# Performance work log

Measured on AMD Instinct MI355X. Metric: run time of the kernel, lower is better.

Reference implementation:

```python
import jax, jax.numpy as jnp
import numpy as np

NB = 8            # num_blocks
D = 128           # embed_dim
D_INNER = 256     # expand=2
HEADS = 4
P = 64            # headdim
N = 32            # d_state
K = 4             # d_conv
CONV_DIM = D_INNER + 2 * N          # 320 (x, B, C streams)
D_IN_PROJ = 2 * D_INNER + 2 * N + HEADS  # 580 (z, xBC, dt)


def setup_inputs():
    key = jax.random.key(0)
    ks = iter(jax.random.split(key, 16))
    f = lambda shape, s=0.02: (jax.random.normal(next(ks), shape, jnp.float32) * s)
    B, L = 2, 4096
    return {
        'x': jax.random.normal(next(ks), (B, L, D), jnp.float32),
        'residual': jnp.zeros((B, L, D), jnp.float32),
        'ln1_w': jnp.ones((NB, D)), 'ln1_b': jnp.zeros((NB, D)),
        'ln2_w': jnp.ones((NB, D)), 'ln2_b': jnp.zeros((NB, D)),
        'fc1_w': f((NB, 4 * D, D)), 'fc1_b': jnp.zeros((NB, 4 * D)),
        'fc2_w': f((NB, D, 2 * D)), 'fc2_b': jnp.zeros((NB, D)),
        'in_proj_w': f((NB, D_IN_PROJ, D)),
        'conv_w': f((NB, CONV_DIM, K), 0.1), 'conv_b': jnp.zeros((NB, CONV_DIM)),
        'dt_bias': f((NB, HEADS), 0.1),
        'A_log': jnp.tile(jnp.log(jnp.arange(1, HEADS + 1, dtype=jnp.float32)), (NB, 1)),
        'Dp': jnp.ones((NB, HEADS)),
        'rms_w': jnp.ones((NB, D_INNER)),
        'out_proj_w': f((NB, D, D_INNER)),
        'h': 64, 'w': 64,
    }


def layernorm(x, w, b):
    mu = jnp.mean(x, -1, keepdims=True)
    var = jnp.mean((x - mu) ** 2, -1, keepdims=True)
    return (x - mu) * jax.lax.rsqrt(var + 1e-5) * w + b


def mamba2(x, in_proj_w, conv_w, conv_b, dt_bias, A_log, Dp, rms_w, out_proj_w):
    Bb, L, _ = x.shape
    zxbcdt = jnp.einsum('bld,ed->ble', x, in_proj_w)          # [B,L,580]
    z = zxbcdt[..., :D_INNER]
    xBC = zxbcdt[..., D_INNER:D_INNER + CONV_DIM]
    dt = jax.nn.softplus(zxbcdt[..., -HEADS:] + dt_bias)      # [B,L,H]
    # causal depthwise conv1d + silu
    xc = jnp.moveaxis(xBC, 1, 2)                              # [B,C,L]
    xc = jax.lax.conv_general_dilated(xc, conv_w[:, None, :], (1,), [(K - 1, 0)],
                                      feature_group_count=CONV_DIM)
    xBC = jax.nn.silu(jnp.moveaxis(xc, 1, 2) + conv_b)
    xs = xBC[..., :D_INNER].reshape(Bb, L, HEADS, P)          # [B,L,H,P]
    Bm = xBC[..., D_INNER:D_INNER + N]                        # [B,L,N]
    Cm = xBC[..., D_INNER + N:]                               # [B,L,N]
    dA = jnp.exp(dt * (-jnp.exp(A_log)))                      # [B,L,H]

    def step(hst, inp):
        dA_t, dt_t, B_t, C_t, x_t = inp
        hst = hst * dA_t[:, :, None, None] + (dt_t[:, :, None, None] * x_t[..., None]) * B_t[:, None, None, :]
        return hst, jnp.einsum('bhpn,bn->bhp', hst, C_t)

    tfirst = lambda a: jnp.moveaxis(a, 1, 0)
    h0 = jnp.zeros((Bb, HEADS, P, N), x.dtype)
    _, ys = jax.lax.scan(step, h0, (tfirst(dA), tfirst(dt), tfirst(Bm), tfirst(Cm), tfirst(xs)))
    y = jnp.moveaxis(ys, 0, 1) + Dp[None, None, :, None] * xs # [B,L,H,P]
    y = y.reshape(Bb, L, D_INNER) * jax.nn.silu(z)            # gated
    y = y * jax.lax.rsqrt(jnp.mean(y * y, -1, keepdims=True) + 1e-5) * rms_w
    return jnp.einsum('be,de->bd'.replace('b', 'bl'), y, out_proj_w)


def mlp(x, fc1_w, fc1_b, fc2_w, fc2_b):
    x12 = jnp.einsum('bld,ed->ble', x, fc1_w) + fc1_b
    x1, x2 = jnp.split(x12, 2, axis=-1)
    return jnp.einsum('ble,de->bld', jax.nn.silu(x1) * x2, fc2_w) + fc2_b


def reference(x, residual, ln1_w, ln1_b, ln2_w, ln2_b, fc1_w, fc1_b, fc2_w, fc2_b,
              in_proj_w, conv_w, conv_b, dt_bias, A_log, Dp, rms_w, out_proj_w, h, w):
    for i in range(NB):
        residual = x
        x1 = layernorm(residual, ln1_w[i], ln1_b[i])
        x_m = residual + mamba2(x1, in_proj_w[i], conv_w[i], conv_b[i], dt_bias[i],
                                A_log[i], Dp[i], rms_w[i], out_proj_w[i])
        residual = x_m
        x2 = layernorm(residual, ln2_w[i], ln2_b[i])
        x = residual + mlp(x2, fc1_w[i], fc1_b[i], fc2_w[i], fc2_b[i])
    return (x, residual)
```

## Files before the change

### kernel.cpp

```cpp
#include <hip/hip_runtime.h>
#include <hip/hip_bf16.h>
#include <cstddef>

#define NBLK 8
#define DD   128
#define DI   256
#define NH   4
#define PP   64
#define NNs  32
#define CONVD 320
#define EE   580
#define BB   2
#define LLEN 4096
#define ML   (BB*LLEN)
#define SEGS 256
#define TT   16
#define GPAD 264

typedef unsigned short u16;
typedef short bf16x8 __attribute__((ext_vector_type(8)));
typedef float f32x4 __attribute__((ext_vector_type(4)));

__device__ __forceinline__ float siluf(float x){ return x / (1.f + expf(-x)); }
__device__ __forceinline__ float b2f(u16 u){ return __uint_as_float((unsigned)u << 16); }
__device__ __forceinline__ u16 f2b(float f){
    __hip_bfloat16 h = __float2bfloat16(f);
    return *reinterpret_cast<u16*>(&h);
}
__device__ __forceinline__ void ld8f(const u16* p, float* f){
    ushort4 a = *(const ushort4*)p;
    ushort4 b = *(const ushort4*)(p + 4);
    f[0]=b2f(a.x); f[1]=b2f(a.y); f[2]=b2f(a.z); f[3]=b2f(a.w);
    f[4]=b2f(b.x); f[5]=b2f(b.y); f[6]=b2f(b.z); f[7]=b2f(b.w);
}

#define IPW_N (NBLK*EE*DD)
#define OPW_N (NBLK*DD*DI)
#define F1W_N (NBLK*512*DD)
#define F2W_N (NBLK*DD*DI)
#define CVT_TOT (IPW_N+OPW_N+F1W_N+F2W_N)

__global__ __launch_bounds__(256) void cvt_weights(const float* __restrict__ ip,
                                                   const float* __restrict__ op,
                                                   const float* __restrict__ f1,
                                                   const float* __restrict__ f2,
                                                   const float* __restrict__ xin,
                                                   u16* __restrict__ dip,
                                                   u16* __restrict__ dop,
                                                   u16* __restrict__ df1,
                                                   u16* __restrict__ df2,
                                                   float* __restrict__ xout)
{
    int i = blockIdx.x * 256 + threadIdx.x;
    if (i < IPW_N)                          dip[i] = f2b(ip[i]);
    else if (i < IPW_N + OPW_N)             dop[i - IPW_N] = f2b(op[i - IPW_N]);
    else if (i < IPW_N + OPW_N + F1W_N)     df1[i - IPW_N - OPW_N] = f2b(f1[i - IPW_N - OPW_N]);
    else                                    df2[i - IPW_N - OPW_N - F1W_N] = f2b(f2[i - IPW_N - OPW_N - F1W_N]);
    if (i < ML * DD) xout[i] = xin[i];
}

__global__ __launch_bounds__(256) void inproj_ln_gemm(const float* __restrict__ X,
                                                      const float* __restrict__ lnw,
                                                      const float* __restrict__ lnb,
                                                      const u16* __restrict__ W,
                                                      u16* __restrict__ C)
{
    __shared__ __align__(16) u16 Ash[64*128];
    __shared__ __align__(16) u16 Wsh[64*128];
    __shared__ float red[64][8];
    const int tid = threadIdx.x;
    const int wave = tid >> 6, lane = tid & 63;
    const int l15 = lane & 15, quad = lane >> 4;
    const int bm = blockIdx.y * 64;
    const int bn = blockIdx.x * 64;
    const int lrow = tid >> 2, sub = tid & 3;

#pragma unroll
    for (int i = 0; i < 4; i++) {
        int k8 = sub + 4*i;
        uint4 wv = make_uint4(0u,0u,0u,0u);
        if (bn + lrow < EE)
            wv = *(const uint4*)(W + (size_t)(bn + lrow) * DD + k8*8);
        *(uint4*)&Wsh[((size_t)k8*64 + lrow) * 8] = wv;
    }

    const float* xr = X + (size_t)(bm + lrow) * DD + sub*32;
    float4 xv[8];
    float ps = 0.f, pq = 0.f;
#pragma unroll
    for (int i = 0; i < 8; i++) {
        xv[i] = *(const float4*)(xr + i*4);
        ps += xv[i].x + xv[i].y + xv[i].z + xv[i].w;
        pq += xv[i].x*xv[i].x + xv[i].y*xv[i].y + xv[i].z*xv[i].z + xv[i].w*xv[i].w;
    }
    red[lrow][sub] = ps; red[lrow][4+sub] = pq;
    __syncthreads();
    float s = red[lrow][0]+red[lrow][1]+red[lrow][2]+red[lrow][3];
    float q = red[lrow][4]+red[lrow][5]+red[lrow][6]+red[lrow][7];
    float mu = s * (1.f/DD);
    float rstd = rsqrtf(q*(1.f/DD) - mu*mu + 1e-5f);
#pragma unroll
    for (int i = 0; i < 4; i++) {
        float4 a0 = xv[2*i], a1 = xv[2*i+1];
        int c0 = sub*32 + i*8;
        u16 o[8];
        o[0] = f2b((a0.x-mu)*rstd*lnw[c0+0] + lnb[c0+0]);
        o[1] = f2b((a0.y-mu)*rstd*lnw[c0+1] + lnb[c0+1]);
        o[2] = f2b((a0.z-mu)*rstd*lnw[c0+2] + lnb[c0+2]);
        o[3] = f2b((a0.w-mu)*rstd*lnw[c0+3] + lnb[c0+3]);
        o[4] = f2b((a1.x-mu)*rstd*lnw[c0+4] + lnb[c0+4]);
        o[5] = f2b((a1.y-mu)*rstd*lnw[c0+5] + lnb[c0+5]);
        o[6] = f2b((a1.z-mu)*rstd*lnw[c0+6] + lnb[c0+6]);
        o[7] = f2b((a1.w-mu)*rstd*lnw[c0+7] + lnb[c0+7]);
        *(uint4*)&Ash[((size_t)(sub*4+i)*64 + lrow) * 8] = *(uint4*)o;
    }
    __syncthreads();

    f32x4 acc[4];
#pragma unroll
    for (int nt = 0; nt < 4; nt++) acc[nt] = (f32x4){0.f,0.f,0.f,0.f};
#pragma unroll
    for (int kk = 0; kk < 4; kk++) {
        bf16x8 af = *(const bf16x8*)&Ash[(((kk*4 + quad)*64) + wave*16 + l15) * 8];
#pragma unroll
        for (int nt = 0; nt < 4; nt++) {
            bf16x8 bfv = *(const bf16x8*)&Wsh[(((kk*4 + quad)*64) + nt*16 + l15) * 8];
            acc[nt] = __builtin_amdgcn_mfma_f32_16x16x32_bf16(af, bfv, acc[nt], 0, 0, 0);
        }
    }
#pragma unroll
    for (int nt = 0; nt < 4; nt++) {
        int n = bn + nt*16 + l15;
        if (n < EE) {
#pragma unroll
            for (int r = 0; r < 4; r++) {
                int m = bm + wave*16 + quad*4 + r;
                C[(size_t)m * EE + n] = f2b(acc[nt][r]);
            }
        }
    }
}

__global__ __launch_bounds__(256) void scan1(const u16* __restrict__ zx,
                                             const float* __restrict__ cw,
                                             const float* __restrict__ cb,
                                             const float* __restrict__ dt_bias,
                                             const float* __restrict__ A_log,
                                             float* __restrict__ seg,
                                             float* __restrict__ segsum)
{
    __shared__ float Bsh[4][TT*NNs];
    __shared__ float dts[4][TT], das[4][TT];
    int wv = threadIdx.x >> 6;
    int p = threadIdx.x & 63;
    int sg = blockIdx.x % (SEGS/4);
    int bh = blockIdx.x / (SEGS/4);
    int h = bh % NH;
    int b = bh / NH;
    int s = sg*4 + wv;
    int l0 = s * TT;
    int row0 = b * LLEN + l0;

    float xr[TT+3];
    const u16* xcol = zx + (size_t)row0 * EE + 256 + h*64 + p;
#pragma unroll
    for (int r = 0; r < TT+3; r++) {
        int l = l0 - 3 + r;
        xr[r] = (l >= 0) ? b2f(xcol[(ptrdiff_t)(r-3) * EE]) : 0.f;
    }
    float4 wx = *(const float4*)(cw + (size_t)(h*64+p) * 4);
    float cbx = cb[h*64+p];

    if (p < NNs) {
        float br[TT+3];
        const u16* bcol = zx + (size_t)row0 * EE + 512 + p;
#pragma unroll
        for (int r = 0; r < TT+3; r++) {
            int l = l0 - 3 + r;
            br[r] = (l >= 0) ? b2f(bcol[(ptrdiff_t)(r-3) * EE]) : 0.f;
        }
        float4 wb = *(const float4*)(cw + (size_t)(256+p) * 4);
        float cbb = cb[256+p];
#pragma unroll
        for (int t = 0; t < TT; t++)
            Bsh[wv][t*NNs + p] = siluf(cbb + wb.x*br[t] + wb.y*br[t+1] + wb.z*br[t+2] + wb.w*br[t+3]);
    }
    if (p < TT) {
        float v = b2f(zx[(size_t)(row0+p)*EE + (EE-NH) + h]) + dt_bias[h];
        float dt = (v > 20.f) ? v : log1pf(expf(v));
        dts[wv][p] = dt;
        das[wv][p] = expf(-expf(A_log[h]) * dt);
    }
    __syncthreads();

    float hreg[NNs];
#pragma unroll
    for (int n = 0; n < NNs; n++) hreg[n] = 0.f;
    float sdt = 0.f;
#pragma unroll
    for (int t = 0; t < TT; t++) {
        float dA = das[wv][t];
        float dt = dts[wv][t];
        float xv = siluf(cbx + wx.x*xr[t] + wx.y*xr[t+1] + wx.z*xr[t+2] + wx.w*xr[t+3]);
        float dtx = dt * xv;
#pragma unroll
        for (int n4 = 0; n4 < 8; n4++) {
            float4 Bv = *(const float4*)&Bsh[wv][t*NNs + n4*4];
            hreg[n4*4+0] = fmaf(hreg[n4*4+0], dA, dtx * Bv.x);
            hreg[n4*4+1] = fmaf(hreg[n4*4+1], dA, dtx * Bv.y);
            hreg[n4*4+2] = fmaf(hreg[n4*4+2], dA, dtx * Bv.z);
            hreg[n4*4+3] = fmaf(hreg[n4*4+3], dA, dtx * Bv.w);
        }
        sdt += dt;
    }
    int bidg = bh * SEGS + s;
    float* dst = seg + ((size_t)bidg * PP + p) * NNs;
#pragma unroll
    for (int n4 = 0; n4 < 8; n4++)
        *(float4*)(dst + n4*4) = make_float4(hreg[n4*4+0], hreg[n4*4+1], hreg[n4*4+2], hreg[n4*4+3]);
    if (p == 0) segsum[bidg] = sdt;
}

__global__ __launch_bounds__(256) void scan2(float* __restrict__ seg,
                                             const float* __restrict__ segsum,
                                             const float* __restrict__ A_log)
{
    int bh = blockIdx.x >> 3;
    int chunk = blockIdx.x & 7;
    int h = bh % NH;
    int entry = chunk * 256 + threadIdx.x;
    float negA = -expf(A_log[h]);
    float hs = 0.f;
    const float* ss = segsum + bh * SEGS;
    float* base = seg + (size_t)bh * SEGS * (PP * NNs) + entry;
    for (int j0 = 0; j0 < SEGS; j0 += 16) {
        float e[16], a[16];
#pragma unroll
        for (int k = 0; k < 16; k++) {
            a[k] = ss[j0 + k];
            e[k] = base[(size_t)(j0 + k) * (PP * NNs)];
        }
#pragma unroll
        for (int k = 0; k < 16; k++) {
            float Aj = expf(negA * a[k]);
            base[(size_t)(j0 + k) * (PP * NNs)] = hs;
            hs = fmaf(Aj, hs, e[k]);
        }
    }
}

__global__ __launch_bounds__(256) void scan3(const u16* __restrict__ zx,
                                             const float* __restrict__ cw,
                                             const float* __restrict__ cb,
                                             const float* __restrict__ dt_bias,
                                             const float* __restrict__ A_log,
                                             const float* __restrict__ seg,
                                             const float* __restrict__ Dp,
                                             u16* __restrict__ y)
{
    __shared__ float BCsh[4][TT*64];
    __shared__ float dts[4][TT], das[4][TT];
    int wv = threadIdx.x >> 6;
    int p = threadIdx.x & 63;
    int sg = blockIdx.x % (SEGS/4);
    int bh = blockIdx.x / (SEGS/4);
    int h = bh % NH;
    int b = bh / NH;
    int s = sg*4 + wv;
    int l0 = s * TT;
    int row0 = b * LLEN + l0;

    float xr[TT+3];
    const u16* xcol = zx + (size_t)row0 * EE + 256 + h*64 + p;
#pragma unroll
    for (int r = 0; r < TT+3; r++) {
        int l = l0 - 3 + r;
        xr[r] = (l >= 0) ? b2f(xcol[(ptrdiff_t)(r-3) * EE]) : 0.f;
    }
    float4 wx = *(const float4*)(cw + (size_t)(h*64+p) * 4);
    float cbx = cb[h*64+p];

    {
        float br[TT+3];
        const u16* bcol = zx + (size_t)row0 * EE + 512 + p;
#pragma unroll
        for (int r = 0; r < TT+3; r++) {
            int l = l0 - 3 + r;
            br[r] = (l >= 0) ? b2f(bcol[(ptrdiff_t)(r-3) * EE]) : 0.f;
        }
        float4 wb = *(const float4*)(cw + (size_t)(256+p) * 4);
        float cbb = cb[256+p];
#pragma unroll
        for (int t = 0; t < TT; t++)
            BCsh[wv][t*64 + p] = siluf(cbb + wb.x*br[t] + wb.y*br[t+1] + wb.z*br[t+2] + wb.w*br[t+3]);
    }
    if (p < TT) {
        float v = b2f(zx[(size_t)(row0+p)*EE + (EE-NH) + h]) + dt_bias[h];
        float dt = (v > 20.f) ? v : log1pf(expf(v));
        dts[wv][p] = dt;
        das[wv][p] = expf(-expf(A_log[h]) * dt);
    }

    float hreg[NNs];
    int bidg = bh * SEGS + s;
    const float* src = seg + ((size_t)bidg * PP + p) * NNs;
#pragma unroll
    for (int n4 = 0; n4 < 8; n4++) {
        float4 v = *(const float4*)(src + n4*4);
        hreg[n4*4+0] = v.x; hreg[n4*4+1] = v.y; hreg[n4*4+2] = v.z; hreg[n4*4+3] = v.w;
    }
    float dp = Dp[h];
    __syncthreads();

#pragma unroll
    for (int t = 0; t < TT; t++) {
        float dA = das[wv][t];
        float dt = dts[wv][t];
        float xv = siluf(cbx + wx.x*xr[t] + wx.y*xr[t+1] + wx.z*xr[t+2] + wx.w*xr[t+3]);
        float dtx = dt * xv;
        float acc = 0.f;
#pragma unroll
        for (int n4 = 0; n4 < 8; n4++) {
            float4 Bv = *(const float4*)&BCsh[wv][t*64 + n4*4];
            float4 Cv = *(const float4*)&BCsh[wv][t*64 + 32 + n4*4];
            hreg[n4*4+0] = fmaf(hreg[n4*4+0], dA, dtx * Bv.x);
            hreg[n4*4+1] = fmaf(hreg[n4*4+1], dA, dtx * Bv.y);
            hreg[n4*4+2] = fmaf(hreg[n4*4+2], dA, dtx * Bv.z);
            hreg[n4*4+3] = fmaf(hreg[n4*4+3], dA, dtx * Bv.w);
            acc = fmaf(hreg[n4*4+0], Cv.x, acc);
            acc = fmaf(hreg[n4*4+1], Cv.y, acc);
            acc = fmaf(hreg[n4*4+2], Cv.z, acc);
            acc = fmaf(hreg[n4*4+3], Cv.w, acc);
        }
        y[(size_t)(row0 + t) * DI + h*PP + p] = f2b(acc + dp * xv);
    }
}

__global__ __launch_bounds__(256) void grms_outproj_gemm(const u16* __restrict__ Y,
                                                         const u16* __restrict__ Z,
                                                         const float* __restrict__ rmsw,
                                                         const u16* __restrict__ W,
                                                         const float* __restrict__ resid,
                                                         float* __restrict__ C)
{
    __shared__ __align__(16) u16 Ash[32*256];
    __shared__ __align__(16) u16 Wsh[64*256];
    __shared__ float red[32][8];
    __shared__ float rl[32];
    const int tid = threadIdx.x;
    const int wave = tid >> 6, lane = tid & 63;
    const int l15 = lane & 15, quad = lane >> 4;
    const int rt = wave & 1, nq = wave >> 1;
    const int bm = blockIdx.y * 32;
    const int bn = blockIdx.x * 64;

    {
        int wrow = tid >> 2, ksub = tid & 3;
#pragma unroll
        for (int i = 0; i < 8; i++) {
            int k8 = ksub + 4*i;
            uint4 wv = *(const uint4*)(W + (size_t)(bn + wrow) * DI + k8*8);
            *(uint4*)&Wsh[((size_t)k8*64 + wrow) * 8] = wv;
        }
    }

    int lrow = tid >> 3, sub = tid & 7;
    const u16* yr = Y + (size_t)(bm + lrow) * DI + sub*32;
    const u16* zr = Z + (size_t)(bm + lrow) * EE + sub*32;
    float pq = 0.f;
#pragma unroll
    for (int i = 0; i < 4; i++) {
        float yv[8], zv[8];
        ld8f(yr + i*8, yv);
        ld8f(zr + i*8, zv);
        int c0 = sub*32 + i*8;
        u16 o[8];
#pragma unroll
        for (int j = 0; j < 8; j++) {
            float g = yv[j] * siluf(zv[j]);
            pq += g*g;
            o[j] = f2b(g * rmsw[c0 + j]);
        }
        *(uint4*)&Ash[((size_t)(sub*4 + i)*32 + lrow) * 8] = *(uint4*)o;
    }
    red[lrow][sub] = pq;
    __syncthreads();
    if (sub == 0) {
        float qq = 0.f;
#pragma unroll
        for (int j = 0; j < 8; j++) qq += red[lrow][j];
        rl[lrow] = rsqrtf(qq * (1.f/DI) + 1e-5f);
    }
    __syncthreads();

    f32x4 acc[2];
    acc[0] = (f32x4){0.f,0.f,0.f,0.f};
    acc[1] = (f32x4){0.f,0.f,0.f,0.f};
#pragma unroll
    for (int kk = 0; kk < 8; kk++) {
        bf16x8 af = *(const bf16x8*)&Ash[(((kk*4 + quad)*32) + rt*16 + l15) * 8];
#pragma unroll
        for (int nt = 0; nt < 2; nt++) {
            bf16x8 bfv = *(const bf16x8*)&Wsh[(((kk*4 + quad)*64) + nq*32 + nt*16 + l15) * 8];
            acc[nt] = __builtin_amdgcn_mfma_f32_16x16x32_bf16(af, bfv, acc[nt], 0, 0, 0);
        }
    }
#pragma unroll
    for (int nt = 0; nt < 2; nt++) {
        int n = bn + nq*32 + nt*16 + l15;
#pragma unroll
        for (int r = 0; r < 4; r++) {
            int lm = rt*16 + quad*4 + r;
            int m = bm + lm;
            C[(size_t)m * DD + n] = acc[nt][r] * rl[lm] + resid[(size_t)m * DD + n];
        }
    }
}

__global__ __launch_bounds__(512) void mlp_fused(const float* __restrict__ Xm,
                                                 const float* __restrict__ lnw,
                                                 const float* __restrict__ lnb,
                                                 const u16* __restrict__ W1,
                                                 const float* __restrict__ b1,
                                                 const u16* __restrict__ W2,
                                                 const float* __restrict__ b2,
                                                 float* __restrict__ Out,
                                                 float* __restrict__ out2)
{
    __shared__ __align__(16) u16 Ash[32*128];
    __shared__ __align__(16) u16 Wsh[128*128];
    __shared__ __align__(16) u16 Gsh[32*GPAD];
    __shared__ float red[32][32];
    const int tid = threadIdx.x;
    const int wv = tid >> 6, lane = tid & 63;
    const int l15 = lane & 15, quad = lane >> 4;
    const int mt = wv & 1, ng = wv >> 1;
    const int bm = blockIdx.x * 32;

    {
        int lrow = tid >> 4, sub = tid & 15;
        const float* xr = Xm + (size_t)(bm + lrow) * DD + sub*8;
        float4 x0 = *(const float4*)xr;
        float4 x1 = *(const float4*)(xr + 4);
        float ps = x0.x+x0.y+x0.z+x0.w + x1.x+x1.y+x1.z+x1.w;
        float pq = x0.x*x0.x+x0.y*x0.y+x0.z*x0.z+x0.w*x0.w
                 + x1.x*x1.x+x1.y*x1.y+x1.z*x1.z+x1.w*x1.w;
        red[lrow][sub] = ps; red[lrow][16+sub] = pq;
        __syncthreads();
        float s = 0.f, q = 0.f;
#pragma unroll
        for (int j = 0; j < 16; j++) { s += red[lrow][j]; q += red[lrow][16+j]; }
        float mu = s * (1.f/DD);
        float rstd = rsqrtf(q*(1.f/DD) - mu*mu + 1e-5f);
        int c0 = sub*8;
        float xa[8] = {x0.x,x0.y,x0.z,x0.w,x1.x,x1.y,x1.z,x1.w};
        u16 o[8];
#pragma unroll
        for (int j = 0; j < 8; j++)
            o[j] = f2b((xa[j]-mu)*rstd*lnw[c0+j] + lnb[c0+j]);
        *(uint4*)&Ash[((size_t)sub*32 + lrow) * 8] = *(uint4*)o;
    }
    __syncthreads();

    bf16x8 afr[4];
#pragma unroll
    for (int kk = 0; kk < 4; kk++)
        afr[kk] = *(const bf16x8*)&Ash[(((kk*4 + quad)*32) + mt*16 + l15) * 8];

    for (int p = 0; p < 4; p++) {
        __syncthreads();
        {
            int wrow = tid >> 2, ksub = tid & 3;
            int r1 = (wrow < 64) ? (p*64 + wrow) : (256 + p*64 + wrow - 64);
#pragma unroll
            for (int i = 0; i < 4; i++) {
                int k8 = ksub + 4*i;
                uint4 wvv = *(const uint4*)(W1 + (size_t)r1 * DD + k8*8);
                *(uint4*)&Wsh[((size_t)k8*128 + wrow) * 8] = wvv;
            }
        }
        __syncthreads();
        f32x4 aa = (f32x4){0.f,0.f,0.f,0.f};
        f32x4 bb = (f32x4){0.f,0.f,0.f,0.f};
#pragma unroll
        for (int kk = 0; kk < 4; kk++) {
            bf16x8 b1v = *(const bf16x8*)&Wsh[(((kk*4 + quad)*128) + ng*16 + l15) * 8];
            bf16x8 b2v = *(const bf16x8*)&Wsh[(((kk*4 + quad)*128) + 64 + ng*16 + l15) * 8];
            aa = __builtin_amdgcn_mfma_f32_16x16x32_bf16(afr[kk], b1v, aa, 0, 0, 0);
            bb = __builtin_amdgcn_mfma_f32_16x16x32_bf16(afr[kk], b2v, bb, 0, 0, 0);
        }
        int n1 = p*64 + ng*16 + l15;
        float ba = b1[n1];
        float bbv = b1[256 + n1];
#pragma unroll
        for (int r = 0; r < 4; r++) {
            float a = aa[r] + ba;
            float bq = bb[r] + bbv;
            int m = mt*16 + quad*4 + r;
            Gsh[m*GPAD + n1] = f2b(siluf(a) * bq);
        }
    }

    f32x4 acc2[2];
    acc2[0] = (f32x4){0.f,0.f,0.f,0.f};
    acc2[1] = (f32x4){0.f,0.f,0.f,0.f};
    for (int kh = 0; kh < 2; kh++) {
        __syncthreads();
        {
            int wrow = tid >> 2, ksub = tid & 3;
#pragma unroll
            for (int i = 0; i < 4; i++) {
                int k8 = ksub + 4*i;
                uint4 wvv = *(const uint4*)(W2 + (size_t)wrow * DI + kh*128 + k8*8);
                *(uint4*)&Wsh[((size_t)k8*128 + wrow) * 8] = wvv;
            }
        }
        __syncthreads();
#pragma unroll
        for (int kk = 0; kk < 4; kk++) {
            bf16x8 af = *(const bf16x8*)&Gsh[(mt*16 + l15)*GPAD + kh*128 + kk*32 + quad*8];
#pragma unroll
            for (int nt = 0; nt < 2; nt++) {
                bf16x8 bfv = *(const bf16x8*)&Wsh[(((kk*4 + quad)*128) + ng*32 + nt*16 + l15) * 8];
                acc2[nt] = __builtin_amdgcn_mfma_f32_16x16x32_bf16(af, bfv, acc2[nt], 0, 0, 0);
            }
        }
    }
#pragma unroll
    for (int nt = 0; nt < 2; nt++) {
        int n = ng*32 + nt*16 + l15;
        float bv = b2[n];
#pragma unroll
        for (int r = 0; r < 4; r++) {
            int m = bm + mt*16 + quad*4 + r;
            float xmv = Xm[(size_t)m * DD + n];
            float v = acc2[nt][r] + bv + xmv;
            Out[(size_t)m * DD + n] = v;
            if (out2) {
                out2[(size_t)m * DD + n] = v;
                out2[(size_t)ML*DD + (size_t)m * DD + n] = xmv;
            }
        }
    }
}

extern "C" void kernel_launch(void* const* d_in, const int* in_sizes, int n_in,
                              void* d_out, int out_size, void* d_ws, size_t ws_size,
                              hipStream_t stream)
{
    (void)in_sizes; (void)n_in; (void)out_size; (void)ws_size;
    const float* x_in      = (const float*)d_in[0];
    const float* ln1_w     = (const float*)d_in[2];
    const float* ln1_b     = (const float*)d_in[3];
    const float* ln2_w     = (const float*)d_in[4];
    const float* ln2_b     = (const float*)d_in[5];
    const float* fc1_w     = (const float*)d_in[6];
    const float* fc1_b     = (const float*)d_in[7];
    const float* fc2_w     = (const float*)d_in[8];
    const float* fc2_b     = (const float*)d_in[9];
    const float* in_proj_w = (const float*)d_in[10];
    const float* conv_w    = (const float*)d_in[11];
    const float* conv_b    = (const float*)d_in[12];
    const float* dt_bias   = (const float*)d_in[13];
    const float* A_log     = (const float*)d_in[14];
    const float* Dp        = (const float*)d_in[15];
    const float* rms_w     = (const float*)d_in[16];
    const float* out_proj_w= (const float*)d_in[17];

    float* ws = (float*)d_ws;
    size_t o = 0;
    float* bufX    = ws + o; o += (size_t)ML * DD;
    float* bufXm   = ws + o; o += (size_t)ML * DD;
    float* bufSeg  = ws + o; o += (size_t)BB * NH * SEGS * PP * NNs;
    float* bufSegA = ws + o; o += (size_t)BB * NH * SEGS;
    u16* bufBigH  = (u16*)(ws + o); o += ((size_t)ML * EE + 1) / 2;
    u16* bufYH    = (u16*)(ws + o); o += (size_t)ML * DI / 2;
    u16* wIpH     = (u16*)(ws + o); o += (IPW_N + 1) / 2;
    u16* wOpH     = (u16*)(ws + o); o += (OPW_N + 1) / 2;
    u16* wF1H     = (u16*)(ws + o); o += (F1W_N + 1) / 2;
    u16* wF2H     = (u16*)(ws + o); o += (F2W_N + 1) / 2;

    cvt_weights<<<CVT_TOT/256, 256, 0, stream>>>(in_proj_w, out_proj_w, fc1_w, fc2_w,
                                                 x_in, wIpH, wOpH, wF1H, wF2H, bufX);

    for (int i = 0; i < NBLK; i++) {
        const float* ln1wi = ln1_w + i * DD;
        const float* ln1bi = ln1_b + i * DD;
        const float* ln2wi = ln2_w + i * DD;
        const float* ln2bi = ln2_b + i * DD;
        const float* cwi   = conv_w + (size_t)i * CONVD * 4;
        const float* cbi   = conv_b + (size_t)i * CONVD;
        const float* dtbi  = dt_bias + i * NH;
        const float* ali   = A_log + i * NH;
        const float* dpi   = Dp + i * NH;
        const float* rwi   = rms_w + (size_t)i * DI;
        const float* f1bi  = fc1_b + (size_t)i * 512;
        const float* f2bi  = fc2_b + (size_t)i * DD;
        const u16* ipwi = wIpH + (size_t)i * EE * DD;
        const u16* opwi = wOpH + (size_t)i * DD * DI;
        const u16* f1wi = wF1H + (size_t)i * 512 * DD;
        const u16* f2wi = wF2H + (size_t)i * DD * DI;

        inproj_ln_gemm<<<dim3(10, ML/64), 256, 0, stream>>>(bufX, ln1wi, ln1bi, ipwi, bufBigH);
        scan1<<<BB*NH*(SEGS/4), 256, 0, stream>>>(bufBigH, cwi, cbi, dtbi, ali, bufSeg, bufSegA);
        scan2<<<BB*NH*8, 256, 0, stream>>>(bufSeg, bufSegA, ali);
        scan3<<<BB*NH*(SEGS/4), 256, 0, stream>>>(bufBigH, cwi, cbi, dtbi, ali, bufSeg, dpi, bufYH);
        grms_outproj_gemm<<<dim3(2, ML/32), 256, 0, stream>>>(bufYH, bufBigH, rwi, opwi,
                                                              bufX, bufXm);
        mlp_fused<<<ML/32, 512, 0, stream>>>(bufXm, ln2wi, ln2bi, f1wi, f1bi,
                                             f2wi, f2bi, bufX,
                                             (i == NBLK-1) ? (float*)d_out : nullptr);
    }
}
```

Baseline: 873.1 us.

## Fuse all layer kernels into one persistent megakernel with grid barriers

Replaces the weight-conversion kernel and the six per-layer kernel launches with a single persistent kernel of 256 blocks. The blocks loop over each stage's tiles in grid-stride fashion and meet at an atomic-counter grid barrier between stages. The aim is to remove per-launch overhead and the gaps between roughly fifty dependent launches. In exchange it runs only one 256-thread block per CU, which lowers occupancy and latency hiding in memory-bound stages. It also adds spin-wait barrier cost and depends on all blocks being co-resident at once.

```diff
diff --git a/kernel.cpp b/kernel.cpp
--- a/kernel.cpp
+++ b/kernel.cpp
@@ -8,7 +8,6 @@
 #define NH   4
 #define PP   64
 #define NNs  32
-#define CONVD 320
 #define EE   580
 #define BB   2
 #define LLEN 4096
@@ -16,6 +15,7 @@
 #define SEGS 256
 #define TT   16
 #define GPAD 264
+#define NB2  256
 
 typedef unsigned short u16;
 typedef short bf16x8 __attribute__((ext_vector_type(8)));
@@ -34,513 +34,533 @@
     f[4]=b2f(b.x); f[5]=b2f(b.y); f[6]=b2f(b.z); f[7]=b2f(b.w);
 }
 
+__device__ __forceinline__ void gsync(unsigned* cnt, unsigned* gen)
+{
+    __syncthreads();
+    if (threadIdx.x == 0) {
+        __threadfence();
+        unsigned g = __hip_atomic_load(gen, __ATOMIC_ACQUIRE, __HIP_MEMORY_SCOPE_AGENT);
+        if (__hip_atomic_fetch_add(cnt, 1u, __ATOMIC_ACQ_REL, __HIP_MEMORY_SCOPE_AGENT) == (NB2 - 1u)) {
+            __hip_atomic_store(cnt, 0u, __ATOMIC_RELAXED, __HIP_MEMORY_SCOPE_AGENT);
+            __hip_atomic_fetch_add(gen, 1u, __ATOMIC_RELEASE, __HIP_MEMORY_SCOPE_AGENT);
+        } else {
+            while (__hip_atomic_load(gen, __ATOMIC_ACQUIRE, __HIP_MEMORY_SCOPE_AGENT) == g)
+                __builtin_amdgcn_s_sleep(4);
+        }
+        __threadfence();
+    }
+    __syncthreads();
+}
+
 #define IPW_N (NBLK*EE*DD)
 #define OPW_N (NBLK*DD*DI)
 #define F1W_N (NBLK*512*DD)
 #define F2W_N (NBLK*DD*DI)
 #define CVT_TOT (IPW_N+OPW_N+F1W_N+F2W_N)
 
-__global__ __launch_bounds__(256) void cvt_weights(const float* __restrict__ ip,
-                                                   const float* __restrict__ op,
-                                                   const float* __restrict__ f1,
-                                                   const float* __restrict__ f2,
-                                                   const float* __restrict__ xin,
-                                                   u16* __restrict__ dip,
-                                                   u16* __restrict__ dop,
-                                                   u16* __restrict__ df1,
-                                                   u16* __restrict__ df2,
-                                                   float* __restrict__ xout)
+struct Params {
+    const float *x_in, *ln1_w, *ln1_b, *ln2_w, *ln2_b;
+    const float *fc1_w, *fc1_b, *fc2_w, *fc2_b;
+    const float *in_proj_w, *conv_w, *conv_b, *dt_bias, *A_log, *Dp, *rms_w, *out_proj_w;
+    float *bufX, *bufXm, *seg, *segsum;
+    u16 *bufBigH, *bufYH, *wIp, *wOp, *wF1, *wF2;
+    float *out;
+    unsigned *barCnt, *barGen;
+};
+
+#define SMEM_BYTES 50304
+
+__global__ __launch_bounds__(256) void mega(Params P)
 {
-    int i = blockIdx.x * 256 + threadIdx.x;
-    if (i < IPW_N)                          dip[i] = f2b(ip[i]);
-    else if (i < IPW_N + OPW_N)             dop[i - IPW_N] = f2b(op[i - IPW_N]);
-    else if (i < IPW_N + OPW_N + F1W_N)     df1[i - IPW_N - OPW_N] = f2b(f1[i - IPW_N - OPW_N]);
-    else                                    df2[i - IPW_N - OPW_N - F1W_N] = f2b(f2[i - IPW_N - OPW_N - F1W_N]);
-    if (i < ML * DD) xout[i] = xin[i];
-}
-
-__global__ __launch_bounds__(256) void inproj_ln_gemm(const float* __restrict__ X,
-                                                      const float* __restrict__ lnw,
-                                                      const float* __restrict__ lnb,
-                                                      const u16* __restrict__ W,
-                                                      u16* __restrict__ C)
-{
-    __shared__ __align__(16) u16 Ash[64*128];
-    __shared__ __align__(16) u16 Wsh[64*128];
-    __shared__ float red[64][8];
+    __shared__ __align__(16) unsigned char smem[SMEM_BYTES];
+    const int bid = blockIdx.x;
     const int tid = threadIdx.x;
     const int wave = tid >> 6, lane = tid & 63;
     const int l15 = lane & 15, quad = lane >> 4;
-    const int bm = blockIdx.y * 64;
-    const int bn = blockIdx.x * 64;
-    const int lrow = tid >> 2, sub = tid & 3;
-
-#pragma unroll
-    for (int i = 0; i < 4; i++) {
-        int k8 = sub + 4*i;
-        uint4 wv = make_uint4(0u,0u,0u,0u);
-        if (bn + lrow < EE)
-            wv = *(const uint4*)(W + (size_t)(bn + lrow) * DD + k8*8);
-        *(uint4*)&Wsh[((size_t)k8*64 + lrow) * 8] = wv;
+
+    for (int j = bid; j < CVT_TOT/256; j += NB2) {
+        int i = j*256 + tid;
+        if (i < IPW_N)                       P.wIp[i] = f2b(P.in_proj_w[i]);
+        else if (i < IPW_N+OPW_N)            P.wOp[i-IPW_N] = f2b(P.out_proj_w[i-IPW_N]);
+        else if (i < IPW_N+OPW_N+F1W_N)      P.wF1[i-IPW_N-OPW_N] = f2b(P.fc1_w[i-IPW_N-OPW_N]);
+        else                                 P.wF2[i-IPW_N-OPW_N-F1W_N] = f2b(P.fc2_w[i-IPW_N-OPW_N-F1W_N]);
+        if (i < ML*DD) P.bufX[i] = P.x_in[i];
     }
-
-    const float* xr = X + (size_t)(bm + lrow) * DD + sub*32;
-    float4 xv[8];
-    float ps = 0.f, pq = 0.f;
-#pragma unroll
-    for (int i = 0; i < 8; i++) {
-        xv[i] = *(const float4*)(xr + i*4);
-        ps += xv[i].x + xv[i].y + xv[i].z + xv[i].w;
-        pq += xv[i].x*xv[i].x + xv[i].y*xv[i].y + xv[i].z*xv[i].z + xv[i].w*xv[i].w;
-    }
-    red[lrow][sub] = ps; red[lrow][4+sub] = pq;
-    __syncthreads();
-    float s = red[lrow][0]+red[lrow][1]+red[lrow][2]+red[lrow][3];
-    float q = red[lrow][4]+red[lrow][5]+red[lrow][6]+red[lrow][7];
-    float mu = s * (1.f/DD);
-    float rstd = rsqrtf(q*(1.f/DD) - mu*mu + 1e-5f);
-#pragma unroll
-    for (int i = 0; i < 4; i++) {
-        float4 a0 = xv[2*i], a1 = xv[2*i+1];
-        int c0 = sub*32 + i*8;
-        u16 o[8];
-        o[0] = f2b((a0.x-mu)*rstd*lnw[c0+0] + lnb[c0+0]);
-        o[1] = f2b((a0.y-mu)*rstd*lnw[c0+1] + lnb[c0+1]);
-        o[2] = f2b((a0.z-mu)*rstd*lnw[c0+2] + lnb[c0+2]);
-        o[3] = f2b((a0.w-mu)*rstd*lnw[c0+3] + lnb[c0+3]);
-        o[4] = f2b((a1.x-mu)*rstd*lnw[c0+4] + lnb[c0+4]);
-        o[5] = f2b((a1.y-mu)*rstd*lnw[c0+5] + lnb[c0+5]);
-        o[6] = f2b((a1.z-mu)*rstd*lnw[c0+6] + lnb[c0+6]);
-        o[7] = f2b((a1.w-mu)*rstd*lnw[c0+7] + lnb[c0+7]);
-        *(uint4*)&Ash[((size_t)(sub*4+i)*64 + lrow) * 8] = *(uint4*)o;
-    }
-    __syncthreads();
-
-    f32x4 acc[4];
-#pragma unroll
-    for (int nt = 0; nt < 4; nt++) acc[nt] = (f32x4){0.f,0.f,0.f,0.f};
-#pragma unroll
-    for (int kk = 0; kk < 4; kk++) {
-        bf16x8 af = *(const bf16x8*)&Ash[(((kk*4 + quad)*64) + wave*16 + l15) * 8];
-#pragma unroll
-        for (int nt = 0; nt < 4; nt++) {
-            bf16x8 bfv = *(const bf16x8*)&Wsh[(((kk*4 + quad)*64) + nt*16 + l15) * 8];
-            acc[nt] = __builtin_amdgcn_mfma_f32_16x16x32_bf16(af, bfv, acc[nt], 0, 0, 0);
-        }
-    }
-#pragma unroll
-    for (int nt = 0; nt < 4; nt++) {
-        int n = bn + nt*16 + l15;
-        if (n < EE) {
-#pragma unroll
-            for (int r = 0; r < 4; r++) {
-                int m = bm + wave*16 + quad*4 + r;
-                C[(size_t)m * EE + n] = f2b(acc[nt][r]);
+    gsync(P.barCnt, P.barGen);
+
+#pragma unroll 1
+    for (int layer = 0; layer < NBLK; layer++) {
+        const float* ln1w = P.ln1_w + layer*DD;
+        const float* ln1b = P.ln1_b + layer*DD;
+        const float* ln2w = P.ln2_w + layer*DD;
+        const float* ln2b = P.ln2_b + layer*DD;
+        const float* cw   = P.conv_w + (size_t)layer*320*4;
+        const float* cb   = P.conv_b + (size_t)layer*320;
+        const float* dtb  = P.dt_bias + layer*NH;
+        const float* alog = P.A_log + layer*NH;
+        const float* dp_  = P.Dp + layer*NH;
+        const float* rmsw = P.rms_w + (size_t)layer*DI;
+        const float* f1b  = P.fc1_b + (size_t)layer*512;
+        const float* f2b_ = P.fc2_b + (size_t)layer*DD;
+        const u16* ipw = P.wIp + (size_t)layer*EE*DD;
+        const u16* opw = P.wOp + (size_t)layer*DD*DI;
+        const u16* f1w = P.wF1 + (size_t)layer*512*DD;
+        const u16* f2w = P.wF2 + (size_t)layer*DD*DI;
+
+        {
+            u16* Ash = (u16*)smem;
+            u16* Wsh = (u16*)(smem + 16384);
+            float (*red)[8] = (float(*)[8])(smem + 32768);
+            const int lrow = tid >> 2, sub = tid & 3;
+#pragma unroll 1
+            for (int tile = bid; tile < 10*(ML/64); tile += NB2) {
+                int by = tile / 10, bx = tile % 10;
+                int bm = by * 64, bn = bx * 64;
+#pragma unroll
+                for (int i = 0; i < 4; i++) {
+                    int k8 = sub + 4*i;
+                    uint4 wv = make_uint4(0u,0u,0u,0u);
+                    if (bn + lrow < EE)
+                        wv = *(const uint4*)(ipw + (size_t)(bn + lrow)*DD + k8*8);
+                    *(uint4*)&Wsh[((size_t)k8*64 + lrow)*8] = wv;
+                }
+                const float* xr = P.bufX + (size_t)(bm + lrow)*DD + sub*32;
+                float4 xv[8];
+                float ps = 0.f, pq = 0.f;
+#pragma unroll
+                for (int i = 0; i < 8; i++) {
+                    xv[i] = *(const float4*)(xr + i*4);
+                    ps += xv[i].x + xv[i].y + xv[i].z + xv[i].w;
+                    pq += xv[i].x*xv[i].x + xv[i].y*xv[i].y + xv[i].z*xv[i].z + xv[i].w*xv[i].w;
+                }
+                red[lrow][sub] = ps; red[lrow][4+sub] = pq;
+                __syncthreads();
+                float s = red[lrow][0]+red[lrow][1]+red[lrow][2]+red[lrow][3];
+                float q = red[lrow][4]+red[lrow][5]+red[lrow][6]+red[lrow][7];
+                float mu = s * (1.f/DD);
+                float rstd = rsqrtf(q*(1.f/DD) - mu*mu + 1e-5f);
+#pragma unroll
+                for (int i = 0; i < 4; i++) {
+                    float4 a0 = xv[2*i], a1 = xv[2*i+1];
+                    int c0 = sub*32 + i*8;
+                    u16 o[8];
+                    o[0] = f2b((a0.x-mu)*rstd*ln1w[c0+0] + ln1b[c0+0]);
+                    o[1] = f2b((a0.y-mu)*rstd*ln1w[c0+1] + ln1b[c0+1]);
+                    o[2] = f2b((a0.z-mu)*rstd*ln1w[c0+2] + ln1b[c0+2]);
+                    o[3] = f2b((a0.w-mu)*rstd*ln1w[c0+3] + ln1b[c0+3]);
+                    o[4] = f2b((a1.x-mu)*rstd*ln1w[c0+4] + ln1b[c0+4]);
+                    o[5] = f2b((a1.y-mu)*rstd*ln1w[c0+5] + ln1b[c0+5]);
+                    o[6] = f2b((a1.z-mu)*rstd*ln1w[c0+6] + ln1b[c0+6]);
+                    o[7] = f2b((a1.w-mu)*rstd*ln1w[c0+7] + ln1b[c0+7]);
+                    *(uint4*)&Ash[((size_t)(sub*4+i)*64 + lrow)*8] = *(uint4*)o;
+                }
+                __syncthreads();
+                f32x4 acc[4];
+#pragma unroll
+                for (int nt = 0; nt < 4; nt++) acc[nt] = (f32x4){0.f,0.f,0.f,0.f};
+#pragma unroll
+                for (int kk = 0; kk < 4; kk++) {
+                    bf16x8 af = *(const bf16x8*)&Ash[(((kk*4 + quad)*64) + wave*16 + l15)*8];
+#pragma unroll
+                    for (int nt = 0; nt < 4; nt++) {
+                        bf16x8 bfv = *(const bf16x8*)&Wsh[(((kk*4 + quad)*64) + nt*16 + l15)*8];
+                        acc[nt] = __builtin_amdgcn_mfma_f32_16x16x32_bf16(af, bfv, acc[nt], 0, 0, 0);
+                    }
+                }
+#pragma unroll
+                for (int nt = 0; nt < 4; nt++) {
+                    int n = bn + nt*16 + l15;
+                    if (n < EE) {
+#pragma unroll
+                        for (int r = 0; r < 4; r++) {
+                            int m = bm + wave*16 + quad*4 + r;
+                            P.bufBigH[(size_t)m*EE + n] = f2b(acc[nt][r]);
+                        }
+                    }
+                }
+                __syncthreads();
             }
         }
-    }
-}
-
-__global__ __launch_bounds__(256) void scan1(const u16* __restrict__ zx,
-                                             const float* __restrict__ cw,
-                                             const float* __restrict__ cb,
-                                             const float* __restrict__ dt_bias,
-                                             const float* __restrict__ A_log,
-                                             float* __restrict__ seg,
-                                             float* __restrict__ segsum)
-{
-    __shared__ float Bsh[4][TT*NNs];
-    __shared__ float dts[4][TT], das[4][TT];
-    int wv = threadIdx.x >> 6;
-    int p = threadIdx.x & 63;
-    int sg = blockIdx.x % (SEGS/4);
-    int bh = blockIdx.x / (SEGS/4);
-    int h = bh % NH;
-    int b = bh / NH;
-    int s = sg*4 + wv;
-    int l0 = s * TT;
-    int row0 = b * LLEN + l0;
-
-    float xr[TT+3];
-    const u16* xcol = zx + (size_t)row0 * EE + 256 + h*64 + p;
-#pragma unroll
-    for (int r = 0; r < TT+3; r++) {
-        int l = l0 - 3 + r;
-        xr[r] = (l >= 0) ? b2f(xcol[(ptrdiff_t)(r-3) * EE]) : 0.f;
-    }
-    float4 wx = *(const float4*)(cw + (size_t)(h*64+p) * 4);
-    float cbx = cb[h*64+p];
-
-    if (p < NNs) {
-        float br[TT+3];
-        const u16* bcol = zx + (size_t)row0 * EE + 512 + p;
-#pragma unroll
-        for (int r = 0; r < TT+3; r++) {
-            int l = l0 - 3 + r;
-            br[r] = (l >= 0) ? b2f(bcol[(ptrdiff_t)(r-3) * EE]) : 0.f;
-        }
-        float4 wb = *(const float4*)(cw + (size_t)(256+p) * 4);
-        float cbb = cb[256+p];
-#pragma unroll
-        for (int t = 0; t < TT; t++)
-            Bsh[wv][t*NNs + p] = siluf(cbb + wb.x*br[t] + wb.y*br[t+1] + wb.z*br[t+2] + wb.w*br[t+3]);
-    }
-    if (p < TT) {
-        float v = b2f(zx[(size_t)(row0+p)*EE + (EE-NH) + h]) + dt_bias[h];
-        float dt = (v > 20.f) ? v : log1pf(expf(v));
-        dts[wv][p] = dt;
-        das[wv][p] = expf(-expf(A_log[h]) * dt);
-    }
-    __syncthreads();
-
-    float hreg[NNs];
-#pragma unroll
-    for (int n = 0; n < NNs; n++) hreg[n] = 0.f;
-    float sdt = 0.f;
-#pragma unroll
-    for (int t = 0; t < TT; t++) {
-        float dA = das[wv][t];
-        float dt = dts[wv][t];
-        float xv = siluf(cbx + wx.x*xr[t] + wx.y*xr[t+1] + wx.z*xr[t+2] + wx.w*xr[t+3]);
-        float dtx = dt * xv;
-#pragma unroll
-        for (int n4 = 0; n4 < 8; n4++) {
-            float4 Bv = *(const float4*)&Bsh[wv][t*NNs + n4*4];
-            hreg[n4*4+0] = fmaf(hreg[n4*4+0], dA, dtx * Bv.x);
-            hreg[n4*4+1] = fmaf(hreg[n4*4+1], dA, dtx * Bv.y);
-            hreg[n4*4+2] = fmaf(hreg[n4*4+2], dA, dtx * Bv.z);
-            hreg[n4*4+3] = fmaf(hreg[n4*4+3], dA, dtx * Bv.w);
-        }
-        sdt += dt;
-    }
-    int bidg = bh * SEGS + s;
-    float* dst = seg + ((size_t)bidg * PP + p) * NNs;
-#pragma unroll
-    for (int n4 = 0; n4 < 8; n4++)
-        *(float4*)(dst + n4*4) = make_float4(hreg[n4*4+0], hreg[n4*4+1], hreg[n4*4+2], hreg[n4*4+3]);
-    if (p == 0) segsum[bidg] = sdt;
-}
-
-__global__ __launch_bounds__(256) void scan2(float* __restrict__ seg,
-                                             const float* __restrict__ segsum,
-                                             const float* __restrict__ A_log)
-{
-    int bh = blockIdx.x >> 3;
-    int chunk = blockIdx.x & 7;
-    int h = bh % NH;
-    int entry = chunk * 256 + threadIdx.x;
-    float negA = -expf(A_log[h]);
-    float hs = 0.f;
-    const float* ss = segsum + bh * SEGS;
-    float* base = seg + (size_t)bh * SEGS * (PP * NNs) + entry;
-    for (int j0 = 0; j0 < SEGS; j0 += 16) {
-        float e[16], a[16];
-#pragma unroll
-        for (int k = 0; k < 16; k++) {
-            a[k] = ss[j0 + k];
-            e[k] = base[(size_t)(j0 + k) * (PP * NNs)];
-        }
-#pragma unroll
-        for (int k = 0; k < 16; k++) {
-            float Aj = expf(negA * a[k]);
-            base[(size_t)(j0 + k) * (PP * NNs)] = hs;
-            hs = fmaf(Aj, hs, e[k]);
-        }
-    }
-}
-
-__global__ __launch_bounds__(256) void scan3(const u16* __restrict__ zx,
-                                             const float* __restrict__ cw,
-                                             const float* __restrict__ cb,
-                                             const float* __restrict__ dt_bias,
-                                             const float* __restrict__ A_log,
-                                             const float* __restrict__ seg,
-                                             const float* __restrict__ Dp,
-                                             u16* __restrict__ y)
-{
-    __shared__ float BCsh[4][TT*64];
-    __shared__ float dts[4][TT], das[4][TT];
-    int wv = threadIdx.x >> 6;
-    int p = threadIdx.x & 63;
-    int sg = blockIdx.x % (SEGS/4);
-    int bh = blockIdx.x / (SEGS/4);
-    int h = bh % NH;
-    int b = bh / NH;
-    int s = sg*4 + wv;
-    int l0 = s * TT;
-    int row0 = b * LLEN + l0;
-
-    float xr[TT+3];
-    const u16* xcol = zx + (size_t)row0 * EE + 256 + h*64 + p;
-#pragma unroll
-    for (int r = 0; r < TT+3; r++) {
-        int l = l0 - 3 + r;
-        xr[r] = (l >= 0) ? b2f(xcol[(ptrdiff_t)(r-3) * EE]) : 0.f;
-    }
-    float4 wx = *(const float4*)(cw + (size_t)(h*64+p) * 4);
-    float cbx = cb[h*64+p];
-
-    {
-        float br[TT+3];
-        const u16* bcol = zx + (size_t)row0 * EE + 512 + p;
-#pragma unroll
-        for (int r = 0; r < TT+3; r++) {
-            int l = l0 - 3 + r;
-            br[r] = (l >= 0) ? b2f(bcol[(ptrdiff_t)(r-3) * EE]) : 0.f;
-        }
-        float4 wb = *(const float4*)(cw + (size_t)(256+p) * 4);
-        float cbb = cb[256+p];
-#pragma unroll
-        for (int t = 0; t < TT; t++)
-            BCsh[wv][t*64 + p] = siluf(cbb + wb.x*br[t] + wb.y*br[t+1] + wb.z*br[t+2] + wb.w*br[t+3]);
-    }
-    if (p < TT) {
-        float v = b2f(zx[(size_t)(row0+p)*EE + (EE-NH) + h]) + dt_bias[h];
-        float dt = (v > 20.f) ? v : log1pf(expf(v));
-        dts[wv][p] = dt;
-        das[wv][p] = expf(-expf(A_log[h]) * dt);
-    }
-
-    float hreg[NNs];
-    int bidg = bh * SEGS + s;
-    const float* src = seg + ((size_t)bidg * PP + p) * NNs;
-#pragma unroll
-    for (int n4 = 0; n4 < 8; n4++) {
-        float4 v = *(const float4*)(src + n4*4);
-        hreg[n4*4+0] = v.x; hreg[n4*4+1] = v.y; hreg[n4*4+2] = v.z; hreg[n4*4+3] = v.w;
-    }
-    float dp = Dp[h];
-    __syncthreads();
-
-#pragma unroll
-    for (int t = 0; t < TT; t++) {
-        float dA = das[wv][t];
-        float dt = dts[wv][t];
-        float xv = siluf(cbx + wx.x*xr[t] + wx.y*xr[t+1] + wx.z*xr[t+2] + wx.w*xr[t+3]);
-        float dtx = dt * xv;
-        float acc = 0.f;
-#pragma unroll
-        for (int n4 = 0; n4 < 8; n4++) {
-            float4 Bv = *(const float4*)&BCsh[wv][t*64 + n4*4];
-            float4 Cv = *(const float4*)&BCsh[wv][t*64 + 32 + n4*4];
-            hreg[n4*4+0] = fmaf(hreg[n4*4+0], dA, dtx * Bv.x);
-            hreg[n4*4+1] = fmaf(hreg[n4*4+1], dA, dtx * Bv.y);
-            hreg[n4*4+2] = fmaf(hreg[n4*4+2], dA, dtx * Bv.z);
-            hreg[n4*4+3] = fmaf(hreg[n4*4+3], dA, dtx * Bv.w);
-            acc = fmaf(hreg[n4*4+0], Cv.x, acc);
-            acc = fmaf(hreg[n4*4+1], Cv.y, acc);
-            acc = fmaf(hreg[n4*4+2], Cv.z, acc);
-            acc = fmaf(hreg[n4*4+3], Cv.w, acc);
-        }
-        y[(size_t)(row0 + t) * DI + h*PP + p] = f2b(acc + dp * xv);
-    }
-}
-
-__global__ __launch_bounds__(256) void grms_outproj_gemm(const u16* __restrict__ Y,
-                                                         const u16* __restrict__ Z,
-                                                         const float* __restrict__ rmsw,
-                                                         const u16* __restrict__ W,
-                                                         const float* __restrict__ resid,
-                                                         float* __restrict__ C)
-{
-    __shared__ __align__(16) u16 Ash[32*256];
-    __shared__ __align__(16) u16 Wsh[64*256];
-    __shared__ float red[32][8];
-    __shared__ float rl[32];
-    const int tid = threadIdx.x;
-    const int wave = tid >> 6, lane = tid & 63;
-    const int l15 = lane & 15, quad = lane >> 4;
-    const int rt = wave & 1, nq = wave >> 1;
-    const int bm = blockIdx.y * 32;
-    const int bn = blockIdx.x * 64;
-
-    {
-        int wrow = tid >> 2, ksub = tid & 3;
-#pragma unroll
-        for (int i = 0; i < 8; i++) {
-            int k8 = ksub + 4*i;
-            uint4 wv = *(const uint4*)(W + (size_t)(bn + wrow) * DI + k8*8);
-            *(uint4*)&Wsh[((size_t)k8*64 + wrow) * 8] = wv;
-        }
-    }
-
-    int lrow = tid >> 3, sub = tid & 7;
-    const u16* yr = Y + (size_t)(bm + lrow) * DI + sub*32;
-    const u16* zr = Z + (size_t)(bm + lrow) * EE + sub*32;
-    float pq = 0.f;
-#pragma unroll
-    for (int i = 0; i < 4; i++) {
-        float yv[8], zv[8];
-        ld8f(yr + i*8, yv);
-        ld8f(zr + i*8, zv);
-        int c0 = sub*32 + i*8;
-        u16 o[8];
-#pragma unroll
-        for (int j = 0; j < 8; j++) {
-            float g = yv[j] * siluf(zv[j]);
-            pq += g*g;
-            o[j] = f2b(g * rmsw[c0 + j]);
-        }
-        *(uint4*)&Ash[((size_t)(sub*4 + i)*32 + lrow) * 8] = *(uint4*)o;
-    }
-    red[lrow][sub] = pq;
-    __syncthreads();
-    if (sub == 0) {
-        float qq = 0.f;
-#pragma unroll
-        for (int j = 0; j < 8; j++) qq += red[lrow][j];
-        rl[lrow] = rsqrtf(qq * (1.f/DI) + 1e-5f);
-    }
-    __syncthreads();
-
-    f32x4 acc[2];
-    acc[0] = (f32x4){0.f,0.f,0.f,0.f};
-    acc[1] = (f32x4){0.f,0.f,0.f,0.f};
-#pragma unroll
-    for (int kk = 0; kk < 8; kk++) {
-        bf16x8 af = *(const bf16x8*)&Ash[(((kk*4 + quad)*32) + rt*16 + l15) * 8];
-#pragma unroll
-        for (int nt = 0; nt < 2; nt++) {
-            bf16x8 bfv = *(const bf16x8*)&Wsh[(((kk*4 + quad)*64) + nq*32 + nt*16 + l15) * 8];
-            acc[nt] = __builtin_amdgcn_mfma_f32_16x16x32_bf16(af, bfv, acc[nt], 0, 0, 0);
-        }
-    }
-#pragma unroll
-    for (int nt = 0; nt < 2; nt++) {
-        int n = bn + nq*32 + nt*16 + l15;
-#pragma unroll
-        for (int r = 0; r < 4; r++) {
-            int lm = rt*16 + quad*4 + r;
-            int m = bm + lm;
-            C[(size_t)m * DD + n] = acc[nt][r] * rl[lm] + resid[(size_t)m * DD + n];
-        }
-    }
-}
-
-__global__ __launch_bounds__(512) void mlp_fused(const float* __restrict__ Xm,
-                                                 const float* __restrict__ lnw,
-                                                 const float* __restrict__ lnb,
-                                                 const u16* __restrict__ W1,
-                                                 const float* __restrict__ b1,
-                                                 const u16* __restrict__ W2,
-                                                 const float* __restrict__ b2,
-                                                 float* __restrict__ Out,
-                                                 float* __restrict__ out2)
-{
-    __shared__ __align__(16) u16 Ash[32*128];
-    __shared__ __align__(16) u16 Wsh[128*128];
-    __shared__ __align__(16) u16 Gsh[32*GPAD];
-    __shared__ float red[32][32];
-    const int tid = threadIdx.x;
-    const int wv = tid >> 6, lane = tid & 63;
-    const int l15 = lane & 15, quad = lane >> 4;
-    const int mt = wv & 1, ng = wv >> 1;
-    const int bm = blockIdx.x * 32;
-
-    {
-        int lrow = tid >> 4, sub = tid & 15;
-        const float* xr = Xm + (size_t)(bm + lrow) * DD + sub*8;
-        float4 x0 = *(const float4*)xr;
-        float4 x1 = *(const float4*)(xr + 4);
-        float ps = x0.x+x0.y+x0.z+x0.w + x1.x+x1.y+x1.z+x1.w;
-        float pq = x0.x*x0.x+x0.y*x0.y+x0.z*x0.z+x0.w*x0.w
-                 + x1.x*x1.x+x1.y*x1.y+x1.z*x1.z+x1.w*x1.w;
-        red[lrow][sub] = ps; red[lrow][16+sub] = pq;
-        __syncthreads();
-        float s = 0.f, q = 0.f;
-#pragma unroll
-        for (int j = 0; j < 16; j++) { s += red[lrow][j]; q += red[lrow][16+j]; }
-        float mu = s * (1.f/DD);
-        float rstd = rsqrtf(q*(1.f/DD) - mu*mu + 1e-5f);
-        int c0 = sub*8;
-        float xa[8] = {x0.x,x0.y,x0.z,x0.w,x1.x,x1.y,x1.z,x1.w};
-        u16 o[8];
-#pragma unroll
-        for (int j = 0; j < 8; j++)
-            o[j] = f2b((xa[j]-mu)*rstd*lnw[c0+j] + lnb[c0+j]);
-        *(uint4*)&Ash[((size_t)sub*32 + lrow) * 8] = *(uint4*)o;
-    }
-    __syncthreads();
-
-    bf16x8 afr[4];
-#pragma unroll
-    for (int kk = 0; kk < 4; kk++)
-        afr[kk] = *(const bf16x8*)&Ash[(((kk*4 + quad)*32) + mt*16 + l15) * 8];
-
-    for (int p = 0; p < 4; p++) {
-        __syncthreads();
+        gsync(P.barCnt, P.barGen);
+
         {
-            int wrow = tid >> 2, ksub = tid & 3;
-            int r1 = (wrow < 64) ? (p*64 + wrow) : (256 + p*64 + wrow - 64);
-#pragma unroll
-            for (int i = 0; i < 4; i++) {
-                int k8 = ksub + 4*i;
-                uint4 wvv = *(const uint4*)(W1 + (size_t)r1 * DD + k8*8);
-                *(uint4*)&Wsh[((size_t)k8*128 + wrow) * 8] = wvv;
+            float* Bsh = (float*)smem;
+            float* dts = (float*)(smem + 8192);
+            float* das = (float*)(smem + 8448);
+#pragma unroll 1
+            for (int u = bid; u < 512; u += NB2) {
+                int wv = wave;
+                int p = lane;
+                int sg = u % (SEGS/4);
+                int bh = u / (SEGS/4);
+                int h = bh % NH;
+                int b = bh / NH;
+                int s = sg*4 + wv;
+                int l0 = s * TT;
+                int row0 = b * LLEN + l0;
+
+                float xr[TT+3];
+                const u16* xcol = P.bufBigH + (size_t)row0*EE + 256 + h*64 + p;
+#pragma unroll
+                for (int r = 0; r < TT+3; r++) {
+                    int l = l0 - 3 + r;
+                    xr[r] = (l >= 0) ? b2f(xcol[(ptrdiff_t)(r-3)*EE]) : 0.f;
+                }
+                float4 wx = *(const float4*)(cw + (size_t)(h*64+p)*4);
+                float cbx = cb[h*64+p];
+                if (p < NNs) {
+                    float br[TT+3];
+                    const u16* bcol = P.bufBigH + (size_t)row0*EE + 512 + p;
+#pragma unroll
+                    for (int r = 0; r < TT+3; r++) {
+                        int l = l0 - 3 + r;
+                        br[r] = (l >= 0) ? b2f(bcol[(ptrdiff_t)(r-3)*EE]) : 0.f;
+                    }
+                    float4 wb = *(const float4*)(cw + (size_t)(256+p)*4);
+                    float cbb = cb[256+p];
+#pragma unroll
+                    for (int t = 0; t < TT; t++)
+                        Bsh[wv*512 + t*NNs + p] = siluf(cbb + wb.x*br[t] + wb.y*br[t+1] + wb.z*br[t+2] + wb.w*br[t+3]);
+                }
+                if (p < TT) {
+                    float v = b2f(P.bufBigH[(size_t)(row0+p)*EE + (EE-NH) + h]) + dtb[h];
+                    float dt = (v > 20.f) ? v : log1pf(expf(v));
+                    dts[wv*16 + p] = dt;
+                    das[wv*16 + p] = expf(-expf(alog[h]) * dt);
+                }
+                __syncthreads();
+
+                float hreg[NNs];
+#pragma unroll
+                for (int n = 0; n < NNs; n++) hreg[n] = 0.f;
+                float sdt = 0.f;
+#pragma unroll
+                for (int t = 0; t < TT; t++) {
+                    float dA = das[wv*16 + t];
+                    float dt = dts[wv*16 + t];
+                    float xv = siluf(cbx + wx.x*xr[t] + wx.y*xr[t+1] + wx.z*xr[t+2] + wx.w*xr[t+3]);
+                    float dtx = dt * xv;
+#pragma unroll
+                    for (int n4 = 0; n4 < 8; n4++) {
+                        float4 Bv = *(const float4*)&Bsh[wv*512 + t*NNs + n4*4];
+                        hreg[n4*4+0] = fmaf(hreg[n4*4+0], dA, dtx * Bv.x);
+                        hreg[n4*4+1] = fmaf(hreg[n4*4+1], dA, dtx * Bv.y);
+                        hreg[n4*4+2] = fmaf(hreg[n4*4+2], dA, dtx * Bv.z);
+                        hreg[n4*4+3] = fmaf(hreg[n4*4+3], dA, dtx * Bv.w);
+                    }
+                    sdt += dt;
+                }
+                int bidg = bh * SEGS + s;
+                float* dst = P.seg + ((size_t)bidg*PP + p)*NNs;
+#pragma unroll
+                for (int n4 = 0; n4 < 8; n4++)
+                    *(float4*)(dst + n4*4) = make_float4(hreg[n4*4+0], hreg[n4*4+1], hreg[n4*4+2], hreg[n4*4+3]);
+                if (p == 0) P.segsum[bidg] = sdt;
+                __syncthreads();
             }
         }
-        __syncthreads();
-        f32x4 aa = (f32x4){0.f,0.f,0.f,0.f};
-        f32x4 bb = (f32x4){0.f,0.f,0.f,0.f};
-#pragma unroll
-        for (int kk = 0; kk < 4; kk++) {
-            bf16x8 b1v = *(const bf16x8*)&Wsh[(((kk*4 + quad)*128) + ng*16 + l15) * 8];
-            bf16x8 b2v = *(const bf16x8*)&Wsh[(((kk*4 + quad)*128) + 64 + ng*16 + l15) * 8];
-            aa = __builtin_amdgcn_mfma_f32_16x16x32_bf16(afr[kk], b1v, aa, 0, 0, 0);
-            bb = __builtin_amdgcn_mfma_f32_16x16x32_bf16(afr[kk], b2v, bb, 0, 0, 0);
-        }
-        int n1 = p*64 + ng*16 + l15;
-        float ba = b1[n1];
-        float bbv = b1[256 + n1];
-#pragma unroll
-        for (int r = 0; r < 4; r++) {
-            float a = aa[r] + ba;
-            float bq = bb[r] + bbv;
-            int m = mt*16 + quad*4 + r;
-            Gsh[m*GPAD + n1] = f2b(siluf(a) * bq);
-        }
-    }
-
-    f32x4 acc2[2];
-    acc2[0] = (f32x4){0.f,0.f,0.f,0.f};
-    acc2[1] = (f32x4){0.f,0.f,0.f,0.f};
-    for (int kh = 0; kh < 2; kh++) {
-        __syncthreads();
-        {
-            int wrow = tid >> 2, ksub = tid & 3;
-#pragma unroll
-            for (int i = 0; i < 4; i++) {
-                int k8 = ksub + 4*i;
-                uint4 wvv = *(const uint4*)(W2 + (size_t)wrow * DI + kh*128 + k8*8);
-                *(uint4*)&Wsh[((size_t)k8*128 + wrow) * 8] = wvv;
+        gsync(P.barCnt, P.barGen);
+
+        if (bid < 64) {
+            int bh = bid >> 3;
+            int chunk = bid & 7;
+            int h = bh % NH;
+            int entry = chunk*256 + tid;
+            float negA = -expf(alog[h]);
+            float hs = 0.f;
+            const float* ss = P.segsum + bh*SEGS;
+            float* base = P.seg + (size_t)bh*SEGS*(PP*NNs) + entry;
+            for (int j0 = 0; j0 < SEGS; j0 += 16) {
+                float e[16], a[16];
+#pragma unroll
+                for (int k = 0; k < 16; k++) {
+                    a[k] = ss[j0 + k];
+                    e[k] = base[(size_t)(j0 + k)*(PP*NNs)];
+                }
+#pragma unroll
+                for (int k = 0; k < 16; k++) {
+                    float Aj = expf(negA * a[k]);
+                    base[(size_t)(j0 + k)*(PP*NNs)] = hs;
+                    hs = fmaf(Aj, hs, e[k]);
+                }
             }
         }
-        __syncthreads();
-#pragma unroll
-        for (int kk = 0; kk < 4; kk++) {
-            bf16x8 af = *(const bf16x8*)&Gsh[(mt*16 + l15)*GPAD + kh*128 + kk*32 + quad*8];
-#pragma unroll
-            for (int nt = 0; nt < 2; nt++) {
-                bf16x8 bfv = *(const bf16x8*)&Wsh[(((kk*4 + quad)*128) + ng*32 + nt*16 + l15) * 8];
-                acc2[nt] = __builtin_amdgcn_mfma_f32_16x16x32_bf16(af, bfv, acc2[nt], 0, 0, 0);
+        gsync(P.barCnt, P.barGen);
+
+        {
+            float* BCsh = (float*)smem;
+            float* dts = (float*)(smem + 16384);
+            float* das = (float*)(smem + 16640);
+#pragma unroll 1
+            for (int u = bid; u < 512; u += NB2) {
+                int wv = wave;
+                int p = lane;
+                int sg = u % (SEGS/4);
+                int bh = u / (SEGS/4);
+                int h = bh % NH;
+                int b = bh / NH;
+                int s = sg*4 + wv;
+                int l0 = s * TT;
+                int row0 = b * LLEN + l0;
+
+                float xr[TT+3];
+                const u16* xcol = P.bufBigH + (size_t)row0*EE + 256 + h*64 + p;
+#pragma unroll
+                for (int r = 0; r < TT+3; r++) {
+                    int l = l0 - 3 + r;
+                    xr[r] = (l >= 0) ? b2f(xcol[(ptrdiff_t)(r-3)*EE]) : 0.f;
+                }
+                float4 wx = *(const float4*)(cw + (size_t)(h*64+p)*4);
+                float cbx = cb[h*64+p];
+                {
+                    float br[TT+3];
+                    const u16* bcol = P.bufBigH + (size_t)row0*EE + 512 + p;
+#pragma unroll
+                    for (int r = 0; r < TT+3; r++) {
+                        int l = l0 - 3 + r;
+                        br[r] = (l >= 0) ? b2f(bcol[(ptrdiff_t)(r-3)*EE]) : 0.f;
+                    }
+                    float4 wb = *(const float4*)(cw + (size_t)(256+p)*4);
+                    float cbb = cb[256+p];
+#pragma unroll
+                    for (int t = 0; t < TT; t++)
+                        BCsh[wv*1024 + t*64 + p] = siluf(cbb + wb.x*br[t] + wb.y*br[t+1] + wb.z*br[t+2] + wb.w*br[t+3]);
+                }
+                if (p < TT) {
+                    float v = b2f(P.bufBigH[(size_t)(row0+p)*EE + (EE-NH) + h]) + dtb[h];
+                    float dt = (v > 20.f) ? v : log1pf(expf(v));
+                    dts[wv*16 + p] = dt;
+                    das[wv*16 + p] = expf(-expf(alog[h]) * dt);
+                }
+                float hreg[NNs];
+                int bidg = bh * SEGS + s;
+                const float* src = P.seg + ((size_t)bidg*PP + p)*NNs;
+#pragma unroll
+                for (int n4 = 0; n4 < 8; n4++) {
+                    float4 v = *(const float4*)(src + n4*4);
+                    hreg[n4*4+0] = v.x; hreg[n4*4+1] = v.y; hreg[n4*4+2] = v.z; hreg[n4*4+3] = v.w;
+                }
+                float dpv = dp_[h];
+                __syncthreads();
+#pragma unroll
+                for (int t = 0; t < TT; t++) {
+                    float dA = das[wv*16 + t];
+                    float dt = dts[wv*16 + t];
+                    float xv = siluf(cbx + wx.x*xr[t] + wx.y*xr[t+1] + wx.z*xr[t+2] + wx.w*xr[t+3]);
+                    float dtx = dt * xv;
+                    float acc = 0.f;
+#pragma unroll
+                    for (int n4 = 0; n4 < 8; n4++) {
+                        float4 Bv = *(const float4*)&BCsh[wv*1024 + t*64 + n4*4];
+                        float4 Cv = *(const float4*)&BCsh[wv*1024 + t*64 + 32 + n4*4];
+                        hreg[n4*4+0] = fmaf(hreg[n4*4+0], dA, dtx * Bv.x);
+                        hreg[n4*4+1] = fmaf(hreg[n4*4+1], dA, dtx * Bv.y);
+                        hreg[n4*4+2] = fmaf(hreg[n4*4+2], dA, dtx * Bv.z);
+                        hreg[n4*4+3] = fmaf(hreg[n4*4+3], dA, dtx * Bv.w);
+                        acc = fmaf(hreg[n4*4+0], Cv.x, acc);
+                        acc = fmaf(hreg[n4*4+1], Cv.y, acc);
+                        acc = fmaf(hreg[n4*4+2], Cv.z, acc);
+                        acc = fmaf(hreg[n4*4+3], Cv.w, acc);
+                    }
+                    P.bufYH[(size_t)(row0 + t)*DI + h*PP + p] = f2b(acc + dpv * xv);
+                }
+                __syncthreads();
             }
         }
-    }
-#pragma unroll
-    for (int nt = 0; nt < 2; nt++) {
-        int n = ng*32 + nt*16 + l15;
-        float bv = b2[n];
-#pragma unroll
-        for (int r = 0; r < 4; r++) {
-            int m = bm + mt*16 + quad*4 + r;
-            float xmv = Xm[(size_t)m * DD + n];
-            float v = acc2[nt][r] + bv + xmv;
-            Out[(size_t)m * DD + n] = v;
-            if (out2) {
-                out2[(size_t)m * DD + n] = v;
-                out2[(size_t)ML*DD + (size_t)m * DD + n] = xmv;
+        gsync(P.barCnt, P.barGen);
+
+        {
+            u16* Ash = (u16*)smem;
+            u16* Wsh = (u16*)(smem + 16384);
+            float (*red)[8] = (float(*)[8])(smem + 49152);
+            float* rl = (float*)(smem + 50176);
+            const int rt = wave & 1, nq = wave >> 1;
+#pragma unroll 1
+            for (int u = bid; u < 512; u += NB2) {
+                int by = u >> 1, bx = u & 1;
+                int bm = by * 32, bn = bx * 64;
+                {
+                    int wrow = tid >> 2, ksub = tid & 3;
+#pragma unroll
+                    for (int i = 0; i < 8; i++) {
+                        int k8 = ksub + 4*i;
+                        *(uint4*)&Wsh[((size_t)k8*64 + wrow)*8] =
+                            *(const uint4*)(opw + (size_t)(bn + wrow)*DI + k8*8);
+                    }
+                }
+                int lrow = tid >> 3, sub = tid & 7;
+                const u16* yr = P.bufYH + (size_t)(bm + lrow)*DI + sub*32;
+                const u16* zr = P.bufBigH + (size_t)(bm + lrow)*EE + sub*32;
+                float pq = 0.f;
+#pragma unroll
+                for (int i = 0; i < 4; i++) {
+                    float yv[8], zv[8];
+                    ld8f(yr + i*8, yv);
+                    ld8f(zr + i*8, zv);
+                    int c0 = sub*32 + i*8;
+                    u16 o[8];
+#pragma unroll
+                    for (int j = 0; j < 8; j++) {
+                        float g = yv[j] * siluf(zv[j]);
+                        pq += g*g;
+                        o[j] = f2b(g * rmsw[c0 + j]);
+                    }
+                    *(uint4*)&Ash[((size_t)(sub*4 + i)*32 + lrow)*8] = *(uint4*)o;
+                }
+                red[lrow][sub] = pq;
+                __syncthreads();
+                if (sub == 0) {
+                    float qq = 0.f;
+#pragma unroll
+                    for (int j = 0; j < 8; j++) qq += red[lrow][j];
+                    rl[lrow] = rsqrtf(qq * (1.f/DI) + 1e-5f);
+                }
+                __syncthreads();
+                f32x4 acc[2];
+                acc[0] = (f32x4){0.f,0.f,0.f,0.f};
+                acc[1] = (f32x4){0.f,0.f,0.f,0.f};
+#pragma unroll
+                for (int kk = 0; kk < 8; kk++) {
+                    bf16x8 af = *(const bf16x8*)&Ash[(((kk*4 + quad)*32) + rt*16 + l15)*8];
+#pragma unroll
+                    for (int nt = 0; nt < 2; nt++) {
+                        bf16x8 bfv = *(const bf16x8*)&Wsh[(((kk*4 + quad)*64) + nq*32 + nt*16 + l15)*8];
+                        acc[nt] = __builtin_amdgcn_mfma_f32_16x16x32_bf16(af, bfv, acc[nt], 0, 0, 0);
+                    }
+                }
+#pragma unroll
+                for (int nt = 0; nt < 2; nt++) {
+                    int n = bn + nq*32 + nt*16 + l15;
+#pragma unroll
+                    for (int r = 0; r < 4; r++) {
+                        int lm = rt*16 + quad*4 + r;
+                        int m = bm + lm;
+                        P.bufXm[(size_t)m*DD + n] = acc[nt][r] * rl[lm] + P.bufX[(size_t)m*DD + n];
+                    }
+                }
+                __syncthreads();
             }
         }
+        gsync(P.barCnt, P.barGen);
+
+        {
+            u16* Ash = (u16*)smem;
+            u16* Wsh = (u16*)(smem + 4096);
+            u16* Gsh = (u16*)(smem + 4096 + 32768);
+            float (*red)[32] = (float(*)[32])(smem + 45312);
+            const int ng = wave;
+#pragma unroll 1
+            for (int u = bid; u < 512; u += NB2) {
+                const int bm = u * 16;
+                {
+                    int lrow = tid >> 4, sub = tid & 15;
+                    const float* xr = P.bufXm + (size_t)(bm + lrow)*DD + sub*8;
+                    float4 x0 = *(const float4*)xr;
+                    float4 x1 = *(const float4*)(xr + 4);
+                    float ps = x0.x+x0.y+x0.z+x0.w + x1.x+x1.y+x1.z+x1.w;
+                    float pq = x0.x*x0.x+x0.y*x0.y+x0.z*x0.z+x0.w*x0.w
+                             + x1.x*x1.x+x1.y*x1.y+x1.z*x1.z+x1.w*x1.w;
+                    red[lrow][sub] = ps; red[lrow][16+sub] = pq;
+                    __syncthreads();
+                    float s = 0.f, q = 0.f;
+#pragma unroll
+                    for (int j = 0; j < 16; j++) { s += red[lrow][j]; q += red[lrow][16+j]; }
+                    float mu = s * (1.f/DD);
+                    float rstd = rsqrtf(q*(1.f/DD) - mu*mu + 1e-5f);
+                    int c0 = sub*8;
+                    float xa[8] = {x0.x,x0.y,x0.z,x0.w,x1.x,x1.y,x1.z,x1.w};
+                    u16 o[8];
+#pragma unroll
+                    for (int j = 0; j < 8; j++)
+                        o[j] = f2b((xa[j]-mu)*rstd*ln2w[c0+j] + ln2b[c0+j]);
+                    *(uint4*)&Ash[((size_t)sub*16 + lrow)*8] = *(uint4*)o;
+                }
+                __syncthreads();
+                bf16x8 afr[4];
+#pragma unroll
+                for (int kk = 0; kk < 4; kk++)
+                    afr[kk] = *(const bf16x8*)&Ash[(((kk*4 + quad)*16) + l15)*8];
+
+#pragma unroll 1
+                for (int p = 0; p < 4; p++) {
+                    __syncthreads();
+                    {
+                        int wrow = tid >> 1, ksub = tid & 1;
+                        int r1 = (wrow < 64) ? (p*64 + wrow) : (256 + p*64 + wrow - 64);
+#pragma unroll
+                        for (int i = 0; i < 8; i++) {
+                            int k8 = ksub + 2*i;
+                            *(uint4*)&Wsh[((size_t)k8*128 + wrow)*8] =
+                                *(const uint4*)(f1w + (size_t)r1*DD + k8*8);
+                        }
+                    }
+                    __syncthreads();
+                    f32x4 aa = (f32x4){0.f,0.f,0.f,0.f};
+                    f32x4 bb = (f32x4){0.f,0.f,0.f,0.f};
+#pragma unroll
+                    for (int kk = 0; kk < 4; kk++) {
+                        bf16x8 b1v = *(const bf16x8*)&Wsh[(((kk*4 + quad)*128) + ng*16 + l15)*8];
+                        bf16x8 b2v = *(const bf16x8*)&Wsh[(((kk*4 + quad)*128) + 64 + ng*16 + l15)*8];
+                        aa = __builtin_amdgcn_mfma_f32_16x16x32_bf16(afr[kk], b1v, aa, 0, 0, 0);
+                        bb = __builtin_amdgcn_mfma_f32_16x16x32_bf16(afr[kk], b2v, bb, 0, 0, 0);
+                    }
+                    int n1 = p*64 + ng*16 + l15;
+                    float ba = f1b[n1];
+                    float bbv = f1b[256 + n1];
+#pragma unroll
+                    for (int r = 0; r < 4; r++) {
+                        float a = aa[r] + ba;
+                        float bq = bb[r] + bbv;
+                        int m = quad*4 + r;
+                        Gsh[m*GPAD + n1] = f2b(siluf(a) * bq);
+                    }
+                }
+                f32x4 acc2[2];
+                acc2[0] = (f32x4){0.f,0.f,0.f,0.f};
+                acc2[1] = (f32x4){0.f,0.f,0.f,0.f};
+#pragma unroll 1
+                for (int kh = 0; kh < 2; kh++) {
+                    __syncthreads();
+                    {
+                        int wrow = tid >> 1, ksub = tid & 1;
+#pragma unroll
+                        for (int i = 0; i < 8; i++) {
+                            int k8 = ksub + 2*i;
+                            *(uint4*)&Wsh[((size_t)k8*128 + wrow)*8] =
+                                *(const uint4*)(f2w + (size_t)wrow*DI + kh*128 + k8*8);
+                        }
+                    }
+                    __syncthreads();
+#pragma unroll
+                    for (int kk = 0; kk < 4; kk++) {
+                        bf16x8 af = *(const bf16x8*)&Gsh[l15*GPAD + kh*128 + kk*32 + quad*8];
+#pragma unroll
+                        for (int nt = 0; nt < 2; nt++) {
+                            bf16x8 bfv = *(const bf16x8*)&Wsh[(((kk*4 + quad)*128) + ng*32 + nt*16 + l15)*8];
+                            acc2[nt] = __builtin_amdgcn_mfma_f32_16x16x32_bf16(af, bfv, acc2[nt], 0, 0, 0);
+                        }
+                    }
+                }
+#pragma unroll
+                for (int nt = 0; nt < 2; nt++) {
+                    int n = ng*32 + nt*16 + l15;
+                    float bv = f2b_[n];
+#pragma unroll
+                    for (int r = 0; r < 4; r++) {
+                        int m = bm + quad*4 + r;
+                        float xmv = P.bufXm[(size_t)m*DD + n];
+                        float v = acc2[nt][r] + bv + xmv;
+                        P.bufX[(size_t)m*DD + n] = v;
+                        if (layer == NBLK-1) {
+                            P.out[(size_t)m*DD + n] = v;
+                            P.out[(size_t)ML*DD + (size_t)m*DD + n] = xmv;
+                        }
+                    }
+                }
+                __syncthreads();
+            }
+        }
+        gsync(P.barCnt, P.barGen);
     }
 }
 
@@ -549,66 +569,42 @@
                               hipStream_t stream)
 {
     (void)in_sizes; (void)n_in; (void)out_size; (void)ws_size;
-    const float* x_in      = (const float*)d_in[0];
-    const float* ln1_w     = (const float*)d_in[2];
-    const float* ln1_b     = (const float*)d_in[3];
-    const float* ln2_w     = (const float*)d_in[4];
-    const float* ln2_b     = (const float*)d_in[5];
-    const float* fc1_w     = (const float*)d_in[6];
-    const float* fc1_b     = (const float*)d_in[7];
-    const float* fc2_w     = (const float*)d_in[8];
-    const float* fc2_b     = (const float*)d_in[9];
-    const float* in_proj_w = (const float*)d_in[10];
-    const float* conv_w    = (const float*)d_in[11];
-    const float* conv_b    = (const float*)d_in[12];
-    const float* dt_bias   = (const float*)d_in[13];
-    const float* A_log     = (const float*)d_in[14];
-    const float* Dp        = (const float*)d_in[15];
-    const float* rms_w     = (const float*)d_in[16];
-    const float* out_proj_w= (const float*)d_in[17];
+    Params prm;
+    prm.x_in      = (const float*)d_in[0];
+    prm.ln1_w     = (const float*)d_in[2];
+    prm.ln1_b     = (const float*)d_in[3];
+    prm.ln2_w     = (const float*)d_in[4];
+    prm.ln2_b     = (const float*)d_in[5];
+    prm.fc1_w     = (const float*)d_in[6];
+    prm.fc1_b     = (const float*)d_in[7];
+    prm.fc2_w     = (const float*)d_in[8];
+    prm.fc2_b     = (const float*)d_in[9];
+    prm.in_proj_w = (const float*)d_in[10];
+    prm.conv_w    = (const float*)d_in[11];
+    prm.conv_b    = (const float*)d_in[12];
+    prm.dt_bias   = (const float*)d_in[13];
+    prm.A_log     = (const float*)d_in[14];
+    prm.Dp        = (const float*)d_in[15];
+    prm.rms_w     = (const float*)d_in[16];
+    prm.out_proj_w= (const float*)d_in[17];
 
     float* ws = (float*)d_ws;
     size_t o = 0;
-    float* bufX    = ws + o; o += (size_t)ML * DD;
-    float* bufXm   = ws + o; o += (size_t)ML * DD;
-    float* bufSeg  = ws + o; o += (size_t)BB * NH * SEGS * PP * NNs;
-    float* bufSegA = ws + o; o += (size_t)BB * NH * SEGS;
-    u16* bufBigH  = (u16*)(ws + o); o += ((size_t)ML * EE + 1) / 2;
-    u16* bufYH    = (u16*)(ws + o); o += (size_t)ML * DI / 2;
-    u16* wIpH     = (u16*)(ws + o); o += (IPW_N + 1) / 2;
-    u16* wOpH     = (u16*)(ws + o); o += (OPW_N + 1) / 2;
-    u16* wF1H     = (u16*)(ws + o); o += (F1W_N + 1) / 2;
-    u16* wF2H     = (u16*)(ws + o); o += (F2W_N + 1) / 2;
-
-    cvt_weights<<<CVT_TOT/256, 256, 0, stream>>>(in_proj_w, out_proj_w, fc1_w, fc2_w,
-                                                 x_in, wIpH, wOpH, wF1H, wF2H, bufX);
-
-    for (int i = 0; i < NBLK; i++) {
-        const float* ln1wi = ln1_w + i * DD;
-        const float* ln1bi = ln1_b + i * DD;
-        const float* ln2wi = ln2_w + i * DD;
-        const float* ln2bi = ln2_b + i * DD;
-        const float* cwi   = conv_w + (size_t)i * CONVD * 4;
-        const float* cbi   = conv_b + (size_t)i * CONVD;
-        const float* dtbi  = dt_bias + i * NH;
-        const float* ali   = A_log + i * NH;
-        const float* dpi   = Dp + i * NH;
-        const float* rwi   = rms_w + (size_t)i * DI;
-        const float* f1bi  = fc1_b + (size_t)i * 512;
-        const float* f2bi  = fc2_b + (size_t)i * DD;
-        const u16* ipwi = wIpH + (size_t)i * EE * DD;
-        const u16* opwi = wOpH + (size_t)i * DD * DI;
-        const u16* f1wi = wF1H + (size_t)i * 512 * DD;
-        const u16* f2wi = wF2H + (size_t)i * DD * DI;
-
-        inproj_ln_gemm<<<dim3(10, ML/64), 256, 0, stream>>>(bufX, ln1wi, ln1bi, ipwi, bufBigH);
-        scan1<<<BB*NH*(SEGS/4), 256, 0, stream>>>(bufBigH, cwi, cbi, dtbi, ali, bufSeg, bufSegA);
-        scan2<<<BB*NH*8, 256, 0, stream>>>(bufSeg, bufSegA, ali);
-        scan3<<<BB*NH*(SEGS/4), 256, 0, stream>>>(bufBigH, cwi, cbi, dtbi, ali, bufSeg, dpi, bufYH);
-        grms_outproj_gemm<<<dim3(2, ML/32), 256, 0, stream>>>(bufYH, bufBigH, rwi, opwi,
-                                                              bufX, bufXm);
-        mlp_fused<<<ML/32, 512, 0, stream>>>(bufXm, ln2wi, ln2bi, f1wi, f1bi,
-                                             f2wi, f2bi, bufX,
-                                             (i == NBLK-1) ? (float*)d_out : nullptr);
-    }
+    prm.bufX   = ws + o; o += (size_t)ML * DD;
+    prm.bufXm  = ws + o; o += (size_t)ML * DD;
+    prm.seg    = ws + o; o += (size_t)BB * NH * SEGS * PP * NNs;
+    prm.segsum = ws + o; o += (size_t)BB * NH * SEGS;
+    prm.bufBigH = (u16*)(ws + o); o += ((size_t)ML * EE + 1) / 2;
+    prm.bufYH   = (u16*)(ws + o); o += (size_t)ML * DI / 2;
+    prm.wIp     = (u16*)(ws + o); o += (IPW_N + 1) / 2;
+    prm.wOp     = (u16*)(ws + o); o += (OPW_N + 1) / 2;
+    prm.wF1     = (u16*)(ws + o); o += (F1W_N + 1) / 2;
+    prm.wF2     = (u16*)(ws + o); o += (F2W_N + 1) / 2;
+    unsigned* bar = (unsigned*)(ws + o); o += 16;
+    prm.barCnt = bar;
+    prm.barGen = bar + 1;
+    prm.out     = (float*)d_out;
+
+    hipMemsetAsync(bar, 0, 2 * sizeof(unsigned), stream);
+    mega<<<dim3(NB2), dim3(256), 0, stream>>>(prm);
 }
```

After: 3.446 ms. 295% more time.
